# Kernel tuning notes

Measured on AMD Instinct MI355X. Metric: run time of the kernel, lower is better.

The kernel has to match this reference:

```python
import jax, jax.numpy as jnp
import numpy as np

# big-endian bit weights for pack/unpack (matches torch packbits/unpackbits bitorder='big')
_BITW = np.array([128, 64, 32, 16, 8, 4, 2, 1], dtype=np.uint8)
_SHIFTS = np.arange(7, -1, -1, dtype=np.uint8)


def _unpackbits(x):
    # x: uint8 [..., n] -> int bits [..., n*8], big-endian
    b = (x[..., None] >> jnp.asarray(_SHIFTS)) & jnp.uint8(1)
    return b.reshape(x.shape[:-1] + (x.shape[-1] * 8,))


def _packbits(bits):
    # bits: bool/int [..., n*8] -> uint8 [..., n], big-endian
    b = bits.astype(jnp.uint8).reshape(bits.shape[:-1] + (bits.shape[-1] // 8, 8))
    return (b * jnp.asarray(_BITW)).sum(axis=-1, dtype=jnp.uint8)


def setup_inputs() -> dict:
    key = jax.random.key(0)
    k1, k2 = jax.random.split(key)
    weights = jax.random.randint(k1, (2048, 256), 0, 256, dtype=jnp.int32).astype(jnp.uint8)
    flip = jax.random.randint(k2, (32, 2048, 256), 0, 256, dtype=jnp.int32).astype(jnp.uint8)
    return {
        "weights": weights,               # bit-packed binary weights [2048, 256] uint8
        "flip": flip,                     # n_votes stacked bit-packed flip votes [32, 2048, 256]
        "n_votes": 32,                    # number of accumulated backward() calls
        "vote_p_max": jnp.array([0.02], dtype=jnp.float32),
    }


def reference(weights, flip, n_votes, vote_p_max):
    # backward(): vote_accumulator += unpackbits(flip), repeated n_votes times
    votes = _unpackbits(flip).astype(jnp.int32).sum(axis=0)   # [2048, 2048] int32
    # update() -> vote2flip(): threshold p = max(vote_p_max, mean/n_votes)
    mean = votes.astype(jnp.float32).mean()
    p = jnp.maximum(vote_p_max[0], mean / n_votes)
    flip_mask = _packbits(votes > p * n_votes)                # [2048, 256] uint8
    # weights = bitwise_xnor(weights, update_mask)
    new_weights = jnp.bitwise_not(jnp.bitwise_xor(weights, flip_mask))
    # calc_1ratio(update_mask): popcount / total bits
    update_ratio = _unpackbits(flip_mask).astype(jnp.float32).mean()
    return new_weights, update_ratio
```

## Files before the change

### kernel.cpp

```cpp
#include <hip/hip_runtime.h>
#include <stdint.h>

typedef unsigned int u32;

__global__ __launch_bounds__(256) void k_count(const int* __restrict__ flip,
                                               u32* __restrict__ planes,
                                               u32* __restrict__ popslot,
                                               int npos, int nvotes) {
    int t = blockIdx.x * blockDim.x + threadIdx.x;
    int pgs = npos >> 2;
    u32 pop = 0;
    if (t < pgs) {
        const int4* fp = (const int4*)flip + t;
        u32 p0 = 0, p1 = 0, p2 = 0, p3 = 0, p4 = 0, p5 = 0;
        int v = 0;
        for (; v + 8 <= nvotes; v += 8) {
            int4 x[8];
#pragma unroll
            for (int j = 0; j < 8; ++j)
                x[j] = fp[(size_t)(v + j) * pgs];
#pragma unroll
            for (int j = 0; j < 8; ++j) {
                u32 w = ((u32)x[j].x & 0xFFu) | (((u32)x[j].y & 0xFFu) << 8)
                      | (((u32)x[j].z & 0xFFu) << 16) | (((u32)x[j].w & 0xFFu) << 24);
                pop += __popc(w);
                u32 c = w, tn;
                tn = p0 & c; p0 ^= c; c = tn;
                tn = p1 & c; p1 ^= c; c = tn;
                tn = p2 & c; p2 ^= c; c = tn;
                tn = p3 & c; p3 ^= c; c = tn;
                tn = p4 & c; p4 ^= c; c = tn;
                p5 ^= c;
            }
        }
        for (; v < nvotes; ++v) {
            int4 x = fp[(size_t)v * pgs];
            u32 w = ((u32)x.x & 0xFFu) | (((u32)x.y & 0xFFu) << 8)
                  | (((u32)x.z & 0xFFu) << 16) | (((u32)x.w & 0xFFu) << 24);
            pop += __popc(w);
            u32 c = w, tn;
            tn = p0 & c; p0 ^= c; c = tn;
            tn = p1 & c; p1 ^= c; c = tn;
            tn = p2 & c; p2 ^= c; c = tn;
            tn = p3 & c; p3 ^= c; c = tn;
            tn = p4 & c; p4 ^= c; c = tn;
            p5 ^= c;
        }
        planes[t]                   = p0;
        planes[(size_t)pgs + t]     = p1;
        planes[(size_t)2*pgs + t]   = p2;
        planes[(size_t)3*pgs + t]   = p3;
        planes[(size_t)4*pgs + t]   = p4;
        planes[(size_t)5*pgs + t]   = p5;
    }
    for (int off = 32; off > 0; off >>= 1)
        pop += __shfl_down(pop, off, 64);
    __shared__ u32 sred[4];
    int wid = threadIdx.x >> 6;
    if ((threadIdx.x & 63) == 0) sred[wid] = pop;
    __syncthreads();
    if (threadIdx.x == 0)
        popslot[blockIdx.x] = sred[0] + sred[1] + sred[2] + sred[3];
}

__global__ __launch_bounds__(256) void k_apply(const int* __restrict__ weights,
                                               const u32* __restrict__ planes,
                                               const u32* __restrict__ popslot,
                                               const float* __restrict__ vote_p_max,
                                               const int* __restrict__ n_votes_p,
                                               float* __restrict__ out,
                                               u32* __restrict__ maskslot,
                                               int npos, int nblk) {
    int pgs = npos >> 2;
    __shared__ u32 sred[4];
    __shared__ float s_thresh;
    u32 s = 0;
    for (int i = threadIdx.x; i < nblk; i += blockDim.x) s += popslot[i];
    for (int off = 32; off > 0; off >>= 1) s += __shfl_down(s, off, 64);
    int wid = threadIdx.x >> 6;
    if ((threadIdx.x & 63) == 0) sred[wid] = s;
    __syncthreads();
    if (threadIdx.x == 0) {
        u32 total = sred[0] + sred[1] + sred[2] + sred[3];
        float nv = (float)n_votes_p[0];
        float mean = (float)((double)total / ((double)npos * 8.0));
        s_thresh = fmaxf(vote_p_max[0] * nv, mean);
    }
    __syncthreads();
    float thresh = s_thresh;
    int t = blockIdx.x * blockDim.x + threadIdx.x;
    u32 pop = 0;
    if (t < pgs) {
        int K = (int)floorf(thresh) + 1;
        if (K < 0) K = 0;
        if (K > 64) K = 64;
        u32 Kp = (u32)(64 - K);
        u32 a0 = planes[t];
        u32 a1 = planes[(size_t)pgs + t];
        u32 a2 = planes[(size_t)2*pgs + t];
        u32 a3 = planes[(size_t)3*pgs + t];
        u32 a4 = planes[(size_t)4*pgs + t];
        u32 a5 = planes[(size_t)5*pgs + t];
        u32 carry = (Kp & 1u)  ? a0 : 0u;
        carry = (Kp & 2u)  ? (a1 | carry) : (a1 & carry);
        carry = (Kp & 4u)  ? (a2 | carry) : (a2 & carry);
        carry = (Kp & 8u)  ? (a3 | carry) : (a3 & carry);
        carry = (Kp & 16u) ? (a4 | carry) : (a4 & carry);
        carry = (Kp & 32u) ? (a5 | carry) : (a5 & carry);
        u32 mask = (K == 0) ? 0xFFFFFFFFu : carry;
        int4 wv = ((const int4*)weights)[t];
        u32 ww = ((u32)wv.x & 0xFFu) | (((u32)wv.y & 0xFFu) << 8)
               | (((u32)wv.z & 0xFFu) << 16) | (((u32)wv.w & 0xFFu) << 24);
        u32 xn = ~(ww ^ mask);
        ((float4*)out)[t] = make_float4((float)(xn & 0xFFu),
                                        (float)((xn >> 8) & 0xFFu),
                                        (float)((xn >> 16) & 0xFFu),
                                        (float)((xn >> 24) & 0xFFu));
        pop = __popc(mask);
    }
    for (int off = 32; off > 0; off >>= 1)
        pop += __shfl_down(pop, off, 64);
    __syncthreads();
    if ((threadIdx.x & 63) == 0) sred[wid] = pop;
    __syncthreads();
    if (threadIdx.x == 0)
        maskslot[blockIdx.x] = sred[0] + sred[1] + sred[2] + sred[3];
}

__global__ __launch_bounds__(256) void k_ratio(const u32* __restrict__ maskslot,
                                               float* __restrict__ out,
                                               int npos, int nblk) {
    __shared__ u32 sred[4];
    u32 s = 0;
    for (int i = threadIdx.x; i < nblk; i += blockDim.x) s += maskslot[i];
    for (int off = 32; off > 0; off >>= 1) s += __shfl_down(s, off, 64);
    int wid = threadIdx.x >> 6;
    if ((threadIdx.x & 63) == 0) sred[wid] = s;
    __syncthreads();
    if (threadIdx.x == 0) {
        u32 mp = sred[0] + sred[1] + sred[2] + sred[3];
        out[npos] = (float)((double)mp / ((double)npos * 8.0));
    }
}

extern "C" void kernel_launch(void* const* d_in, const int* in_sizes, int n_in,
                              void* d_out, int out_size, void* d_ws, size_t ws_size,
                              hipStream_t stream) {
    const int* weights      = (const int*)d_in[0];
    const int* flip         = (const int*)d_in[1];
    const int* n_votes_p    = (const int*)d_in[2];
    const float* vote_p_max = (const float*)d_in[3];

    int npos   = in_sizes[0];
    int nvotes = in_sizes[1] / in_sizes[0];
    int pgs    = npos / 4;

    int block = 256;
    int gx = (pgs + block - 1) / block;

    u32* popslot  = (u32*)d_ws;
    u32* maskslot = (u32*)((char*)d_ws + 16384);
    u32* planes   = (u32*)((char*)d_ws + 65536);

    k_count<<<gx, block, 0, stream>>>(flip, planes, popslot, npos, nvotes);
    k_apply<<<gx, block, 0, stream>>>(weights, planes, popslot, vote_p_max,
                                      n_votes_p, (float*)d_out, maskslot,
                                      npos, gx);
    k_ratio<<<1, block, 0, stream>>>(maskslot, (float*)d_out, npos, gx);
}
```

Measured before the change: 105.8 us.

## Fuse count, apply and ratio kernels into one cooperative kernel with grid sync

Merges the three kernels into one cooperative launch. The bit-plane counters stay in registers across a grid-wide sync instead of being written to and re-read from a workspace buffer. The final update-ratio reduction uses an atomic accumulator with a last-block-done counter rather than a separate single-block kernel. This removes two launches and the plane traffic, at the cost of a grid barrier and requiring every block to be co-resident.

```diff
diff --git a/kernel.cpp b/kernel.cpp
--- a/kernel.cpp
+++ b/kernel.cpp
@@ -1,18 +1,30 @@
 #include <hip/hip_runtime.h>
+#include <hip/hip_cooperative_groups.h>
 #include <stdint.h>
 
+namespace cg = cooperative_groups;
 typedef unsigned int u32;
 
-__global__ __launch_bounds__(256) void k_count(const int* __restrict__ flip,
-                                               u32* __restrict__ planes,
-                                               u32* __restrict__ popslot,
-                                               int npos, int nvotes) {
-    int t = blockIdx.x * blockDim.x + threadIdx.x;
-    int pgs = npos >> 2;
+__global__ __launch_bounds__(256) void k_fused(
+    const int* __restrict__ flip,
+    const int* __restrict__ weights,
+    u32* __restrict__ popslot,
+    u32* __restrict__ acc,
+    const float* __restrict__ vote_p_max,
+    const int* __restrict__ n_votes_p,
+    float* __restrict__ out,
+    int npos, int nvotes, int nblk)
+{
+    cg::grid_group grid = cg::this_grid();
+    const int pgs = npos >> 2;
+    const int t = blockIdx.x * blockDim.x + threadIdx.x;
+
+    if (blockIdx.x == 0 && threadIdx.x == 0) { acc[0] = 0u; acc[1] = 0u; }
+
+    u32 p0 = 0, p1 = 0, p2 = 0, p3 = 0, p4 = 0, p5 = 0;
     u32 pop = 0;
     if (t < pgs) {
         const int4* fp = (const int4*)flip + t;
-        u32 p0 = 0, p1 = 0, p2 = 0, p3 = 0, p4 = 0, p5 = 0;
         int v = 0;
         for (; v + 8 <= nvotes; v += 8) {
             int4 x[8];
@@ -46,38 +58,24 @@
             tn = p4 & c; p4 ^= c; c = tn;
             p5 ^= c;
         }
-        planes[t]                   = p0;
-        planes[(size_t)pgs + t]     = p1;
-        planes[(size_t)2*pgs + t]   = p2;
-        planes[(size_t)3*pgs + t]   = p3;
-        planes[(size_t)4*pgs + t]   = p4;
-        planes[(size_t)5*pgs + t]   = p5;
     }
     for (int off = 32; off > 0; off >>= 1)
         pop += __shfl_down(pop, off, 64);
     __shared__ u32 sred[4];
-    int wid = threadIdx.x >> 6;
+    __shared__ float s_thresh;
+    const int wid = threadIdx.x >> 6;
     if ((threadIdx.x & 63) == 0) sred[wid] = pop;
     __syncthreads();
     if (threadIdx.x == 0)
         popslot[blockIdx.x] = sred[0] + sred[1] + sred[2] + sred[3];
-}
 
-__global__ __launch_bounds__(256) void k_apply(const int* __restrict__ weights,
-                                               const u32* __restrict__ planes,
-                                               const u32* __restrict__ popslot,
-                                               const float* __restrict__ vote_p_max,
-                                               const int* __restrict__ n_votes_p,
-                                               float* __restrict__ out,
-                                               u32* __restrict__ maskslot,
-                                               int npos, int nblk) {
-    int pgs = npos >> 2;
-    __shared__ u32 sred[4];
-    __shared__ float s_thresh;
+    __threadfence();
+    grid.sync();
+    __threadfence();
+
     u32 s = 0;
     for (int i = threadIdx.x; i < nblk; i += blockDim.x) s += popslot[i];
     for (int off = 32; off > 0; off >>= 1) s += __shfl_down(s, off, 64);
-    int wid = threadIdx.x >> 6;
     if ((threadIdx.x & 63) == 0) sred[wid] = s;
     __syncthreads();
     if (threadIdx.x == 0) {
@@ -87,26 +85,20 @@
         s_thresh = fmaxf(vote_p_max[0] * nv, mean);
     }
     __syncthreads();
-    float thresh = s_thresh;
-    int t = blockIdx.x * blockDim.x + threadIdx.x;
-    u32 pop = 0;
+    const float thresh = s_thresh;
+
+    pop = 0;
     if (t < pgs) {
         int K = (int)floorf(thresh) + 1;
         if (K < 0) K = 0;
         if (K > 64) K = 64;
         u32 Kp = (u32)(64 - K);
-        u32 a0 = planes[t];
-        u32 a1 = planes[(size_t)pgs + t];
-        u32 a2 = planes[(size_t)2*pgs + t];
-        u32 a3 = planes[(size_t)3*pgs + t];
-        u32 a4 = planes[(size_t)4*pgs + t];
-        u32 a5 = planes[(size_t)5*pgs + t];
-        u32 carry = (Kp & 1u)  ? a0 : 0u;
-        carry = (Kp & 2u)  ? (a1 | carry) : (a1 & carry);
-        carry = (Kp & 4u)  ? (a2 | carry) : (a2 & carry);
-        carry = (Kp & 8u)  ? (a3 | carry) : (a3 & carry);
-        carry = (Kp & 16u) ? (a4 | carry) : (a4 & carry);
-        carry = (Kp & 32u) ? (a5 | carry) : (a5 & carry);
+        u32 carry = (Kp & 1u)  ? p0 : 0u;
+        carry = (Kp & 2u)  ? (p1 | carry) : (p1 & carry);
+        carry = (Kp & 4u)  ? (p2 | carry) : (p2 & carry);
+        carry = (Kp & 8u)  ? (p3 | carry) : (p3 & carry);
+        carry = (Kp & 16u) ? (p4 | carry) : (p4 & carry);
+        carry = (Kp & 32u) ? (p5 | carry) : (p5 & carry);
         u32 mask = (K == 0) ? 0xFFFFFFFFu : carry;
         int4 wv = ((const int4*)weights)[t];
         u32 ww = ((u32)wv.x & 0xFFu) | (((u32)wv.y & 0xFFu) << 8)
@@ -123,23 +115,16 @@
     __syncthreads();
     if ((threadIdx.x & 63) == 0) sred[wid] = pop;
     __syncthreads();
-    if (threadIdx.x == 0)
-        maskslot[blockIdx.x] = sred[0] + sred[1] + sred[2] + sred[3];
-}
-
-__global__ __launch_bounds__(256) void k_ratio(const u32* __restrict__ maskslot,
-                                               float* __restrict__ out,
-                                               int npos, int nblk) {
-    __shared__ u32 sred[4];
-    u32 s = 0;
-    for (int i = threadIdx.x; i < nblk; i += blockDim.x) s += maskslot[i];
-    for (int off = 32; off > 0; off >>= 1) s += __shfl_down(s, off, 64);
-    int wid = threadIdx.x >> 6;
-    if ((threadIdx.x & 63) == 0) sred[wid] = s;
-    __syncthreads();
     if (threadIdx.x == 0) {
-        u32 mp = sred[0] + sred[1] + sred[2] + sred[3];
-        out[npos] = (float)((double)mp / ((double)npos * 8.0));
+        u32 blockpop = sred[0] + sred[1] + sred[2] + sred[3];
+        atomicAdd(&acc[0], blockpop);
+        __threadfence();
+        u32 old = atomicAdd(&acc[1], 1u);
+        if (old == (u32)(nblk - 1)) {
+            __threadfence();
+            u32 mp = atomicAdd(&acc[0], 0u);
+            out[npos] = (float)((double)mp / ((double)npos * 8.0));
+        }
     }
 }
 
@@ -158,13 +143,13 @@
     int block = 256;
     int gx = (pgs + block - 1) / block;
 
-    u32* popslot  = (u32*)d_ws;
-    u32* maskslot = (u32*)((char*)d_ws + 16384);
-    u32* planes   = (u32*)((char*)d_ws + 65536);
+    u32* popslot = (u32*)d_ws;
+    u32* acc     = (u32*)((char*)d_ws + 16384);
+    float* out_f = (float*)d_out;
 
-    k_count<<<gx, block, 0, stream>>>(flip, planes, popslot, npos, nvotes);
-    k_apply<<<gx, block, 0, stream>>>(weights, planes, popslot, vote_p_max,
-                                      n_votes_p, (float*)d_out, maskslot,
-                                      npos, gx);
-    k_ratio<<<1, block, 0, stream>>>(maskslot, (float*)d_out, npos, gx);
+    void* args[] = { (void*)&flip, (void*)&weights, (void*)&popslot, (void*)&acc,
+                     (void*)&vote_p_max, (void*)&n_votes_p, (void*)&out_f,
+                     (void*)&npos, (void*)&nvotes, (void*)&gx };
+    (void)hipLaunchCooperativeKernel((void*)k_fused, dim3(gx), dim3(block),
+                                     args, 0, stream);
 }
```

New measurement: 240.2 us. 2.27x slower.
